# Kernel tuning notes

Measured on AMD Instinct MI355X. Metric: run time of the kernel, lower is better.

The kernel has to match this reference:

```python
import jax, jax.numpy as jnp
import numpy as np

NX = 65536   # spatial cells
T = 32       # time points
H = 128      # MLP hidden width
DX = 1.0     # spatial resolution (init kwarg dx)
S0, S1 = -1.0, 1.0  # fixed stencil (learn_stencil=False)


def setup_inputs() -> dict:
    key = jax.random.key(0)
    k1, k2, k3, k4 = jax.random.split(key, 4)
    t = jnp.arange(T, dtype=jnp.float32) * 0.01          # time grid, dt=0.01
    u0 = jax.random.uniform(k1, (NX,), jnp.float32)      # initial state
    inv_sqrt_h = jnp.float32(1.0 / np.sqrt(H))
    W1 = jax.random.normal(k2, (1, H), jnp.float32)
    W2 = jax.random.normal(k3, (H, H), jnp.float32) * inv_sqrt_h
    W3 = jax.random.normal(k4, (H, 1), jnp.float32) * inv_sqrt_h
    D = jnp.full((1,), 0.01, jnp.float32)                # diffusion coefficient
    BC = jnp.zeros((2, 1), jnp.float32)                  # Dirichlet BC values
    return {"t": t, "u0": u0, "W1": W1, "W2": W2, "W3": W3, "D": D, "BC": BC}


def _flux(u, W1, W2, W3, D, BC):
    # per-cell MLP (func_nn): Linear->Tanh->Linear->Tanh->Linear, no bias, no sigmoid
    h = jnp.tanh(u[:, None] @ W1)        # [Nx, H]
    h = jnp.tanh(h @ W2)                 # [Nx, H]
    a = (h @ W3)[:, 0]                   # [Nx]
    a_plus = jax.nn.relu(a)
    a_min = -jax.nn.relu(-a)
    d = D[0]
    # left fluxes
    lb = d * (S0 * u[0] + S1 * BC[0, 0]) - a_plus[0] / DX * (-S0 * u[0] - S1 * BC[0, 0])
    ln = d * (S0 * u[1:] + S1 * u[:-1]) - a_plus[1:] / DX * (-S0 * u[1:] - S1 * u[:-1])
    left = jnp.concatenate([lb[None], ln])
    # right fluxes
    rb = d * (S0 * u[-1] + S1 * BC[1, 0]) - a_min[-1] / DX * (S0 * u[-1] + S1 * BC[1, 0])
    rn = d * (S0 * u[:-1] + S1 * u[1:]) - a_min[:-1] / DX * (S0 * u[:-1] + S1 * u[1:])
    right = jnp.concatenate([rn, rb[None]])
    return left + right


def reference(t, u0, W1, W2, W3, D, BC):
    # Neural-ODE integration of du/dt = flux_kernel(u); fixed-step RK4 over grid t
    f = lambda u: _flux(u, W1, W2, W3, D, BC)

    def step(u, dt):
        k1 = f(u)
        k2 = f(u + 0.5 * dt * k1)
        k3 = f(u + 0.5 * dt * k2)
        k4 = f(u + dt * k3)
        un = u + (dt / 6.0) * (k1 + 2.0 * k2 + 2.0 * k3 + k4)
        return un, un

    _, us = jax.lax.scan(step, u0, jnp.diff(t))
    return jnp.concatenate([u0[None], us], axis=0)  # [T, Nx]
```

## Files before the change

### kernel.cpp

```cpp
#include <hip/hip_runtime.h>

#define NXC 65536
#define TT 32
#define HH 128
#define TABN 6145
#define TABNP 6146
#define TABLO (-1.0f)
#define TABINV 2048.0f
#define OUTW 32
#define VC 2
#define WINW 128
#define HALO 48

typedef __attribute__((ext_vector_type(8))) short bf16x8;
typedef __attribute__((ext_vector_type(4))) float f32x4;
typedef unsigned short u16;

__device__ __forceinline__ float bf2f(u16 b) {
    union { unsigned int u; float f; } v; v.u = ((unsigned int)b) << 16; return v.f;
}
__device__ __forceinline__ u16 f2bf(float f) {
    union { float f; unsigned int u; } v; v.f = f;
    return (u16)((v.u + 0x7fffu + ((v.u >> 16) & 1u)) >> 16);
}
__device__ __forceinline__ bool is_bf16_mode(const void* t) {
    return ((const u16*)t)[1] != 0;
}

#if __has_builtin(__builtin_amdgcn_exp2f)
#define EXP2F(x) __builtin_amdgcn_exp2f(x)
#else
#define EXP2F(x) exp2f(x)
#endif
#if __has_builtin(__builtin_amdgcn_rcpf)
#define RCPF(x) __builtin_amdgcn_rcpf(x)
#else
#define RCPF(x) (1.0f / (x))
#endif

__device__ __forceinline__ float fast_tanh(float x) {
    float e = EXP2F(x * 2.8853900817779268f);
    return 1.0f - 2.0f * RCPF(e + 1.0f);
}

__global__ __launch_bounds__(256) void tabbuild_kernel(
    const void* traw, const void* W1, const void* W2, const void* W3,
    float* __restrict__ atab) {
    __shared__ __align__(16) u16 w2s[HH * HH];
    __shared__ float w1s[HH];
    __shared__ float w3s[HH];
    bool bf = is_bf16_mode(traw);
    int tid = threadIdx.x;
    if (tid < HH)
        w1s[tid] = bf ? bf2f(((const u16*)W1)[tid]) : ((const float*)W1)[tid];
    else
        w3s[tid - HH] = bf ? bf2f(((const u16*)W3)[tid - HH])
                           : ((const float*)W3)[tid - HH];
#pragma unroll 4
    for (int it = 0; it < (HH * HH) / 256; ++it) {
        int idx = it * 256 + tid;
        u16 b = bf ? ((const u16*)W2)[idx] : f2bf(((const float*)W2)[idx]);
        int k = idx >> 7, n = idx & 127;
        int frag = ((n >> 4) * 4 + (k >> 5)) * 64 + ((k >> 3) & 3) * 16 + (n & 15);
        w2s[(frag << 3) | (k & 7)] = b;
    }
    __syncthreads();

    int lane = tid & 63;
    int wave = tid >> 6;
    int q = lane >> 4;
    int m = lane & 15;
    int base = (blockIdx.x * 4 + wave) * 16;
    float uin = TABLO + (float)(base + m) * (1.0f / TABINV);

    bf16x8 afrag[4];
#pragma unroll
    for (int ks = 0; ks < 4; ++ks)
#pragma unroll
        for (int j = 0; j < 8; ++j) {
            float h = fast_tanh(uin * w1s[ks * 32 + q * 8 + j]);
            afrag[ks][j] = (short)f2bf(h);
        }

    const bf16x8* w2f = (const bf16x8*)w2s;
    float p0 = 0.f, p1 = 0.f, p2 = 0.f, p3 = 0.f;
#pragma unroll
    for (int nt = 0; nt < 8; ++nt) {
        f32x4 acc = {0.f, 0.f, 0.f, 0.f};
#pragma unroll
        for (int ks = 0; ks < 4; ++ks) {
            bf16x8 b = w2f[(nt * 4 + ks) * 64 + lane];
            acc = __builtin_amdgcn_mfma_f32_16x16x32_bf16(afrag[ks], b, acc, 0, 0, 0);
        }
        float w3v = w3s[nt * 16 + m];
        p0 += fast_tanh(acc[0]) * w3v;
        p1 += fast_tanh(acc[1]) * w3v;
        p2 += fast_tanh(acc[2]) * w3v;
        p3 += fast_tanh(acc[3]) * w3v;
    }
#pragma unroll
    for (int sh = 1; sh < 16; sh <<= 1) {
        p0 += __shfl_xor(p0, sh, 64);
        p1 += __shfl_xor(p1, sh, 64);
        p2 += __shfl_xor(p2, sh, 64);
        p3 += __shfl_xor(p3, sh, 64);
    }
    int r = m & 3;
    float a = (r == 0) ? p0 : (r == 1) ? p1 : (r == 2) ? p2 : p3;
    if (m < 4) {
        int e = base + q * 4 + r;
        if (e < TABNP) atab[e] = a;
    }
}

__global__ __launch_bounds__(256) void chunk_kernel(
    const void* traw, const void* uin, float* __restrict__ uout,
    const void* Draw, const void* BCraw, const float* __restrict__ atab,
    void* outbase, int s0, int nsteps) {
    __shared__ __align__(16) float2 tab[TABN];
    __shared__ float t32s[TT];

    int tid = threadIdx.x;
    bool bf = is_bf16_mode(traw);

    for (int e = tid * 4; e < TABN - 1; e += 1024) {
        float4 qv = *(const float4*)(atab + e);
        float nx = atab[e + 4];
        float4 lo = make_float4(qv.x, qv.y - qv.x, qv.y, qv.z - qv.y);
        float4 hi = make_float4(qv.z, qv.w - qv.z, qv.w, nx - qv.w);
        *(float4*)(&tab[e]) = lo;
        *(float4*)(&tab[e + 2]) = hi;
    }
    if (tid == 0)
        tab[TABN - 1] = make_float2(atab[TABN - 1], atab[TABN] - atab[TABN - 1]);
    if (tid < TT)
        t32s[tid] = bf ? bf2f(((const u16*)traw)[tid]) : ((const float*)traw)[tid];

    float d   = bf ? bf2f(((const u16*)Draw)[0])  : ((const float*)Draw)[0];
    float bc0 = bf ? bf2f(((const u16*)BCraw)[0]) : ((const float*)BCraw)[0];
    float bc1 = bf ? bf2f(((const u16*)BCraw)[1]) : ((const float*)BCraw)[1];

    int lane = tid & 63;
    int wid = blockIdx.x * 4 + (tid >> 6);
    int gb = wid * OUTW - HALO + lane * VC;
    int i0 = lane * VC;
    bool first = (s0 == 0);
    bool ownw = (i0 >= HALO) && (i0 < HALO + OUTW);

    float v[VC], ub[VC], kv[VC], kacc[VC];
    bool gok[VC];
#pragma unroll
    for (int j = 0; j < VC; ++j) {
        int g = gb + j;
        gok[j] = (g >= 0) && (g < NXC);
        float x;
        if (first) {
            if (bf) {
                u16 raw = gok[j] ? ((const u16*)uin)[g] : (u16)0;
                x = bf2f(raw);
                if (ownw) ((u16*)outbase)[g] = raw;
            } else {
                float raw = gok[j] ? ((const float*)uin)[g] : 0.f;
                x = raw;
                if (ownw) ((float*)outbase)[g] = raw;
            }
        } else {
            x = gok[j] ? ((const float*)uin)[g] : 0.f;
        }
        if (!gok[j]) x = (g < 0) ? bc0 : bc1;
        v[j] = x;
        ub[j] = x;
    }
    __syncthreads();

    for (int st = 0; st < nsteps; ++st) {
        int step = s0 + st;
        float dt = t32s[step + 1] - t32s[step];
        float dt2 = 0.5f * dt, dt6 = dt * (1.0f / 6.0f);
#pragma unroll
        for (int j = 0; j < VC; ++j) kacc[j] = 0.f;
#pragma unroll
        for (int s = 0; s < 4; ++s) {
            float cnext = (s < 2) ? dt2 : dt;
            float wgt = (s == 1 || s == 2) ? 2.f : 1.f;
            float vup = __shfl_up(v[VC - 1], 1, 64);
            float vdn = __shfl_down(v[0], 1, 64);
#pragma unroll
            for (int j = 0; j < VC; ++j) {
                float vc = v[j];
                float vl = (j == 0) ? vup : v[j - 1];
                float vr = (j == VC - 1) ? vdn : v[j + 1];
                float f = fmaf(vc, TABINV, (-TABLO) * TABINV);
                f = fminf(fmaxf(f, 0.0f), (float)(TABN - 1));
                int e0 = (int)f;
                float frac = f - (float)e0;
                float2 ts = tab[e0];
                float a = fmaf(frac, ts.y, ts.x);
                float ap = fmaxf(a, 0.f);
                float am = fminf(a, 0.f);
                kv[j] = (vl - vc) * (d + ap) + (vr - vc) * (d - am);
            }
#pragma unroll
            for (int j = 0; j < VC; ++j) {
                kacc[j] += wgt * kv[j];
                float nv = (s < 3) ? fmaf(cnext, kv[j], ub[j])
                                   : fmaf(dt6, kacc[j], ub[j]);
                if (gok[j]) {
                    v[j] = nv;
                    if (s == 3) ub[j] = nv;
                }
            }
        }
        long long rb = (long long)(step + 1) * NXC + gb;
        if (ownw) {
            if (bf) {
                unsigned int pk = (unsigned int)f2bf(ub[0])
                                | ((unsigned int)f2bf(ub[1]) << 16);
                *(unsigned int*)&((u16*)outbase)[rb] = pk;
            } else {
                *(float2*)&((float*)outbase)[rb] = make_float2(ub[0], ub[1]);
            }
        }
    }
    if (uout != nullptr && ownw)
        *(float2*)&uout[gb] = make_float2(ub[0], ub[1]);
}

extern "C" void kernel_launch(void* const* d_in, const int* in_sizes, int n_in,
                              void* d_out, int out_size, void* d_ws,
                              size_t ws_size, hipStream_t stream) {
    const void* t  = d_in[0];
    const void* u0 = d_in[1];
    const void* W1 = d_in[2];
    const void* W2 = d_in[3];
    const void* W3 = d_in[4];
    const void* Dp = d_in[5];
    const void* BC = d_in[6];

    float* atab = (float*)d_ws;
    float* uA = atab + TABNP + 2;
    float* uB = uA + NXC;

    tabbuild_kernel<<<(TABNP + 63) / 64, 256, 0, stream>>>(t, W1, W2, W3, atab);

    const int grid = NXC / (OUTW * 4);
    chunk_kernel<<<grid, 256, 0, stream>>>(t, u0, uB, Dp, BC, atab, d_out, 0, 12);
    chunk_kernel<<<grid, 256, 0, stream>>>(t, uB, uA, Dp, BC, atab, d_out, 12, 12);
    chunk_kernel<<<grid, 256, 0, stream>>>(t, uA, nullptr, Dp, BC, atab, d_out, 24, 7);
}
```

Before: 118.3 us.

## Fuse table build and all RK4 steps into one cooperative kernel

Replaces the table-build kernel and three chunked RK4 kernels with a single cooperative launch. Two grid-wide syncs separate the W2 fragment swizzle (now staged through global memory), the table build and the time stepping. The halo grows to 128 cells per side so all 31 steps run without exchanging state between blocks, with 5 cells per lane and 64 owned outputs per wave. This removes three kernel launches and the intermediate state round-trips, at the cost of more redundant halo computation, more registers, and element-wise rather than vectorised output stores.

```diff
diff --git a/kernel.cpp b/kernel.cpp
--- a/kernel.cpp
+++ b/kernel.cpp
@@ -1,4 +1,7 @@
 #include <hip/hip_runtime.h>
+#include <hip/hip_cooperative_groups.h>
+
+namespace cg = cooperative_groups;
 
 #define NXC 65536
 #define TT 32
@@ -7,10 +10,13 @@
 #define TABNP 6146
 #define TABLO (-1.0f)
 #define TABINV 2048.0f
-#define OUTW 32
-#define VC 2
-#define WINW 128
-#define HALO 48
+#define OUTW 64
+#define VC 5
+#define WINW 320
+#define HALO 128
+#define NSTEPS 31
+#define SWZB 64
+#define TABB 97
 
 typedef __attribute__((ext_vector_type(8))) short bf16x8;
 typedef __attribute__((ext_vector_type(4))) float f32x4;
@@ -43,85 +49,118 @@
     return 1.0f - 2.0f * RCPF(e + 1.0f);
 }
 
-__global__ __launch_bounds__(256) void tabbuild_kernel(
-    const void* traw, const void* W1, const void* W2, const void* W3,
-    float* __restrict__ atab) {
-    __shared__ __align__(16) u16 w2s[HH * HH];
+__global__ __launch_bounds__(256) void mega_kernel(
+    const void* traw, const void* u0, const void* W1, const void* W2,
+    const void* W3, const void* Draw, const void* BCraw,
+    u16* __restrict__ w2frag, float* __restrict__ atab,
+    void* __restrict__ outbase) {
+    __shared__ __align__(16) float2 tab[TABN];
+    __shared__ float t32s[TT];
     __shared__ float w1s[HH];
     __shared__ float w3s[HH];
+
+    int tid = threadIdx.x;
     bool bf = is_bf16_mode(traw);
-    int tid = threadIdx.x;
-    if (tid < HH)
-        w1s[tid] = bf ? bf2f(((const u16*)W1)[tid]) : ((const float*)W1)[tid];
-    else
-        w3s[tid - HH] = bf ? bf2f(((const u16*)W3)[tid - HH])
-                           : ((const float*)W3)[tid - HH];
-#pragma unroll 4
-    for (int it = 0; it < (HH * HH) / 256; ++it) {
-        int idx = it * 256 + tid;
-        u16 b = bf ? ((const u16*)W2)[idx] : f2bf(((const float*)W2)[idx]);
-        int k = idx >> 7, n = idx & 127;
-        int frag = ((n >> 4) * 4 + (k >> 5)) * 64 + ((k >> 3) & 3) * 16 + (n & 15);
-        w2s[(frag << 3) | (k & 7)] = b;
-    }
-    __syncthreads();
-
     int lane = tid & 63;
     int wave = tid >> 6;
-    int q = lane >> 4;
-    int m = lane & 15;
-    int base = (blockIdx.x * 4 + wave) * 16;
-    float uin = TABLO + (float)(base + m) * (1.0f / TABINV);
-
-    bf16x8 afrag[4];
-#pragma unroll
-    for (int ks = 0; ks < 4; ++ks)
-#pragma unroll
-        for (int j = 0; j < 8; ++j) {
-            float h = fast_tanh(uin * w1s[ks * 32 + q * 8 + j]);
-            afrag[ks][j] = (short)f2bf(h);
-        }
-
-    const bf16x8* w2f = (const bf16x8*)w2s;
-    float p0 = 0.f, p1 = 0.f, p2 = 0.f, p3 = 0.f;
-#pragma unroll
-    for (int nt = 0; nt < 8; ++nt) {
-        f32x4 acc = {0.f, 0.f, 0.f, 0.f};
-#pragma unroll
-        for (int ks = 0; ks < 4; ++ks) {
-            bf16x8 b = w2f[(nt * 4 + ks) * 64 + lane];
-            acc = __builtin_amdgcn_mfma_f32_16x16x32_bf16(afrag[ks], b, acc, 0, 0, 0);
-        }
-        float w3v = w3s[nt * 16 + m];
-        p0 += fast_tanh(acc[0]) * w3v;
-        p1 += fast_tanh(acc[1]) * w3v;
-        p2 += fast_tanh(acc[2]) * w3v;
-        p3 += fast_tanh(acc[3]) * w3v;
-    }
-#pragma unroll
-    for (int sh = 1; sh < 16; sh <<= 1) {
-        p0 += __shfl_xor(p0, sh, 64);
-        p1 += __shfl_xor(p1, sh, 64);
-        p2 += __shfl_xor(p2, sh, 64);
-        p3 += __shfl_xor(p3, sh, 64);
-    }
-    int r = m & 3;
-    float a = (r == 0) ? p0 : (r == 1) ? p1 : (r == 2) ? p2 : p3;
-    if (m < 4) {
-        int e = base + q * 4 + r;
-        if (e < TABNP) atab[e] = a;
-    }
-}
-
-__global__ __launch_bounds__(256) void chunk_kernel(
-    const void* traw, const void* uin, float* __restrict__ uout,
-    const void* Draw, const void* BCraw, const float* __restrict__ atab,
-    void* outbase, int s0, int nsteps) {
-    __shared__ __align__(16) float2 tab[TABN];
-    __shared__ float t32s[TT];
-
-    int tid = threadIdx.x;
-    bool bf = is_bf16_mode(traw);
+    int wid = blockIdx.x * 4 + wave;
+    int gb = wid * OUTW - HALO + lane * VC;
+    int i0 = lane * VC;
+
+    float d   = bf ? bf2f(((const u16*)Draw)[0])  : ((const float*)Draw)[0];
+    float bc0 = bf ? bf2f(((const u16*)BCraw)[0]) : ((const float*)BCraw)[0];
+    float bc1 = bf ? bf2f(((const u16*)BCraw)[1]) : ((const float*)BCraw)[1];
+
+    float v[VC], ub[VC];
+    bool gok[VC], own[VC];
+#pragma unroll
+    for (int j = 0; j < VC; ++j) {
+        int g = gb + j;
+        int i = i0 + j;
+        gok[j] = (g >= 0) && (g < NXC);
+        own[j] = (i >= HALO) && (i < HALO + OUTW);
+        float x;
+        if (bf) {
+            u16 raw = gok[j] ? ((const u16*)u0)[g] : (u16)0;
+            x = bf2f(raw);
+            if (own[j]) ((u16*)outbase)[g] = raw;
+        } else {
+            float raw = gok[j] ? ((const float*)u0)[g] : 0.f;
+            x = raw;
+            if (own[j]) ((float*)outbase)[g] = raw;
+        }
+        if (!gok[j]) x = (g < 0) ? bc0 : bc1;
+        v[j] = x;
+        ub[j] = x;
+    }
+
+    if (blockIdx.x < SWZB) {
+        int i = blockIdx.x * 256 + tid;
+        int ej = i & 7;
+        int ln = (i >> 3) & 63;
+        int ks = (i >> 9) & 3;
+        int nt = i >> 11;
+        int k = ks * 32 + (ln >> 4) * 8 + ej;
+        int n = nt * 16 + (ln & 15);
+        w2frag[i] = bf ? ((const u16*)W2)[k * HH + n]
+                       : f2bf(((const float*)W2)[k * HH + n]);
+    }
+    cg::this_grid().sync();
+
+    if (blockIdx.x < TABB) {
+        if (tid < HH)
+            w1s[tid] = bf ? bf2f(((const u16*)W1)[tid]) : ((const float*)W1)[tid];
+        else
+            w3s[tid - HH] = bf ? bf2f(((const u16*)W3)[tid - HH])
+                               : ((const float*)W3)[tid - HH];
+        __syncthreads();
+
+        int q = lane >> 4;
+        int m = lane & 15;
+        int base = (blockIdx.x * 4 + wave) * 16;
+        float uin = TABLO + (float)(base + m) * (1.0f / TABINV);
+
+        bf16x8 afrag[4];
+#pragma unroll
+        for (int ks = 0; ks < 4; ++ks)
+#pragma unroll
+            for (int j = 0; j < 8; ++j) {
+                float h = fast_tanh(uin * w1s[ks * 32 + q * 8 + j]);
+                afrag[ks][j] = (short)f2bf(h);
+            }
+
+        const bf16x8* w2f = (const bf16x8*)w2frag;
+        float p0 = 0.f, p1 = 0.f, p2 = 0.f, p3 = 0.f;
+#pragma unroll
+        for (int nt = 0; nt < 8; ++nt) {
+            f32x4 acc = {0.f, 0.f, 0.f, 0.f};
+#pragma unroll
+            for (int ks = 0; ks < 4; ++ks) {
+                bf16x8 b = w2f[(nt * 4 + ks) * 64 + lane];
+                acc = __builtin_amdgcn_mfma_f32_16x16x32_bf16(afrag[ks], b, acc,
+                                                              0, 0, 0);
+            }
+            float w3v = w3s[nt * 16 + m];
+            p0 += fast_tanh(acc[0]) * w3v;
+            p1 += fast_tanh(acc[1]) * w3v;
+            p2 += fast_tanh(acc[2]) * w3v;
+            p3 += fast_tanh(acc[3]) * w3v;
+        }
+#pragma unroll
+        for (int sh = 1; sh < 16; sh <<= 1) {
+            p0 += __shfl_xor(p0, sh, 64);
+            p1 += __shfl_xor(p1, sh, 64);
+            p2 += __shfl_xor(p2, sh, 64);
+            p3 += __shfl_xor(p3, sh, 64);
+        }
+        int r = m & 3;
+        float a = (r == 0) ? p0 : (r == 1) ? p1 : (r == 2) ? p2 : p3;
+        if (m < 4) {
+            int e = base + q * 4 + r;
+            if (e < TABNP) atab[e] = a;
+        }
+    }
+    cg::this_grid().sync();
 
     for (int e = tid * 4; e < TABN - 1; e += 1024) {
         float4 qv = *(const float4*)(atab + e);
@@ -135,48 +174,12 @@
         tab[TABN - 1] = make_float2(atab[TABN - 1], atab[TABN] - atab[TABN - 1]);
     if (tid < TT)
         t32s[tid] = bf ? bf2f(((const u16*)traw)[tid]) : ((const float*)traw)[tid];
-
-    float d   = bf ? bf2f(((const u16*)Draw)[0])  : ((const float*)Draw)[0];
-    float bc0 = bf ? bf2f(((const u16*)BCraw)[0]) : ((const float*)BCraw)[0];
-    float bc1 = bf ? bf2f(((const u16*)BCraw)[1]) : ((const float*)BCraw)[1];
-
-    int lane = tid & 63;
-    int wid = blockIdx.x * 4 + (tid >> 6);
-    int gb = wid * OUTW - HALO + lane * VC;
-    int i0 = lane * VC;
-    bool first = (s0 == 0);
-    bool ownw = (i0 >= HALO) && (i0 < HALO + OUTW);
-
-    float v[VC], ub[VC], kv[VC], kacc[VC];
-    bool gok[VC];
-#pragma unroll
-    for (int j = 0; j < VC; ++j) {
-        int g = gb + j;
-        gok[j] = (g >= 0) && (g < NXC);
-        float x;
-        if (first) {
-            if (bf) {
-                u16 raw = gok[j] ? ((const u16*)uin)[g] : (u16)0;
-                x = bf2f(raw);
-                if (ownw) ((u16*)outbase)[g] = raw;
-            } else {
-                float raw = gok[j] ? ((const float*)uin)[g] : 0.f;
-                x = raw;
-                if (ownw) ((float*)outbase)[g] = raw;
-            }
-        } else {
-            x = gok[j] ? ((const float*)uin)[g] : 0.f;
-        }
-        if (!gok[j]) x = (g < 0) ? bc0 : bc1;
-        v[j] = x;
-        ub[j] = x;
-    }
     __syncthreads();
 
-    for (int st = 0; st < nsteps; ++st) {
-        int step = s0 + st;
-        float dt = t32s[step + 1] - t32s[step];
+    for (int st = 0; st < NSTEPS; ++st) {
+        float dt = t32s[st + 1] - t32s[st];
         float dt2 = 0.5f * dt, dt6 = dt * (1.0f / 6.0f);
+        float kacc[VC], kv[VC];
 #pragma unroll
         for (int j = 0; j < VC; ++j) kacc[j] = 0.f;
 #pragma unroll
@@ -211,19 +214,18 @@
                 }
             }
         }
-        long long rb = (long long)(step + 1) * NXC + gb;
-        if (ownw) {
-            if (bf) {
-                unsigned int pk = (unsigned int)f2bf(ub[0])
-                                | ((unsigned int)f2bf(ub[1]) << 16);
-                *(unsigned int*)&((u16*)outbase)[rb] = pk;
-            } else {
-                *(float2*)&((float*)outbase)[rb] = make_float2(ub[0], ub[1]);
-            }
-        }
-    }
-    if (uout != nullptr && ownw)
-        *(float2*)&uout[gb] = make_float2(ub[0], ub[1]);
+        if (bf) {
+            u16* orow = (u16*)outbase + (size_t)(st + 1) * NXC;
+#pragma unroll
+            for (int j = 0; j < VC; ++j)
+                if (own[j]) orow[gb + j] = f2bf(ub[j]);
+        } else {
+            float* orow = (float*)outbase + (size_t)(st + 1) * NXC;
+#pragma unroll
+            for (int j = 0; j < VC; ++j)
+                if (own[j]) orow[gb + j] = ub[j];
+        }
+    }
 }
 
 extern "C" void kernel_launch(void* const* d_in, const int* in_sizes, int n_in,
@@ -238,13 +240,14 @@
     const void* BC = d_in[6];
 
     float* atab = (float*)d_ws;
-    float* uA = atab + TABNP + 2;
-    float* uB = uA + NXC;
-
-    tabbuild_kernel<<<(TABNP + 63) / 64, 256, 0, stream>>>(t, W1, W2, W3, atab);
+    u16* w2frag = (u16*)(atab + TABNP + 2);
+    void* outb = d_out;
+
+    void* kargs[] = {(void*)&t,  (void*)&u0, (void*)&W1, (void*)&W2,
+                     (void*)&W3, (void*)&Dp, (void*)&BC, (void*)&w2frag,
+                     (void*)&atab, (void*)&outb};
 
     const int grid = NXC / (OUTW * 4);
-    chunk_kernel<<<grid, 256, 0, stream>>>(t, u0, uB, Dp, BC, atab, d_out, 0, 12);
-    chunk_kernel<<<grid, 256, 0, stream>>>(t, uB, uA, Dp, BC, atab, d_out, 12, 12);
-    chunk_kernel<<<grid, 256, 0, stream>>>(t, uA, nullptr, Dp, BC, atab, d_out, 24, 7);
-}
+    hipLaunchCooperativeKernel((void*)mega_kernel, dim3(grid), dim3(256),
+                               kargs, 0, stream);
+}
```

After: 181.2 us. 53.2% more time.

## Widen chunk window to block-level with LDS edge exchange, fewer chunk launches

Applied to the files above, without the earlier changes.

The chunk kernel now treats a whole 256-thread block as one window, with one cell per thread: 128 owned cells and a 64-cell halo on each side. Cells at wave edges are passed between waves through shared memory, with a __syncthreads on every RK stage. This cuts the number of time chunks from three launches to two (16+15 steps) and lowers halo overhead per owned cell. The table-build kernel also stops staging W2 in LDS and reads its fragments straight from global memory. The trade-off is per-stage block barriers and scalar stores where there were paired vector stores.

```diff
diff --git a/kernel.cpp b/kernel.cpp
--- a/kernel.cpp
+++ b/kernel.cpp
@@ -7,10 +7,9 @@
 #define TABNP 6146
 #define TABLO (-1.0f)
 #define TABINV 2048.0f
-#define OUTW 32
-#define VC 2
-#define WINW 128
-#define HALO 48
+#define OWNB 128
+#define WINB 256
+#define HALOB 64
 
 typedef __attribute__((ext_vector_type(8))) short bf16x8;
 typedef __attribute__((ext_vector_type(4))) float f32x4;
@@ -46,7 +45,6 @@
 __global__ __launch_bounds__(256) void tabbuild_kernel(
     const void* traw, const void* W1, const void* W2, const void* W3,
     float* __restrict__ atab) {
-    __shared__ __align__(16) u16 w2s[HH * HH];
     __shared__ float w1s[HH];
     __shared__ float w3s[HH];
     bool bf = is_bf16_mode(traw);
@@ -56,14 +54,6 @@
     else
         w3s[tid - HH] = bf ? bf2f(((const u16*)W3)[tid - HH])
                            : ((const float*)W3)[tid - HH];
-#pragma unroll 4
-    for (int it = 0; it < (HH * HH) / 256; ++it) {
-        int idx = it * 256 + tid;
-        u16 b = bf ? ((const u16*)W2)[idx] : f2bf(((const float*)W2)[idx]);
-        int k = idx >> 7, n = idx & 127;
-        int frag = ((n >> 4) * 4 + (k >> 5)) * 64 + ((k >> 3) & 3) * 16 + (n & 15);
-        w2s[(frag << 3) | (k & 7)] = b;
-    }
     __syncthreads();
 
     int lane = tid & 63;
@@ -82,14 +72,20 @@
             afrag[ks][j] = (short)f2bf(h);
         }
 
-    const bf16x8* w2f = (const bf16x8*)w2s;
+    const u16* w2u = (const u16*)W2;
+    const float* w2ff = (const float*)W2;
     float p0 = 0.f, p1 = 0.f, p2 = 0.f, p3 = 0.f;
 #pragma unroll
     for (int nt = 0; nt < 8; ++nt) {
         f32x4 acc = {0.f, 0.f, 0.f, 0.f};
 #pragma unroll
         for (int ks = 0; ks < 4; ++ks) {
-            bf16x8 b = w2f[(nt * 4 + ks) * 64 + lane];
+            int idx0 = (ks * 32 + q * 8) * HH + nt * 16 + m;
+            bf16x8 b;
+#pragma unroll
+            for (int j = 0; j < 8; ++j)
+                b[j] = bf ? (short)w2u[idx0 + j * HH]
+                          : (short)f2bf(w2ff[idx0 + j * HH]);
             acc = __builtin_amdgcn_mfma_f32_16x16x32_bf16(afrag[ks], b, acc, 0, 0, 0);
         }
         float w3v = w3s[nt * 16 + m];
@@ -116,9 +112,11 @@
 __global__ __launch_bounds__(256) void chunk_kernel(
     const void* traw, const void* uin, float* __restrict__ uout,
     const void* Draw, const void* BCraw, const float* __restrict__ atab,
-    void* outbase, int s0, int nsteps) {
+    void* __restrict__ outbase, int s0, int nsteps) {
     __shared__ __align__(16) float2 tab[TABN];
     __shared__ float t32s[TT];
+    __shared__ float eL[2][4];
+    __shared__ float eR[2][4];
 
     int tid = threadIdx.x;
     bool bf = is_bf16_mode(traw);
@@ -141,35 +139,31 @@
     float bc1 = bf ? bf2f(((const u16*)BCraw)[1]) : ((const float*)BCraw)[1];
 
     int lane = tid & 63;
-    int wid = blockIdx.x * 4 + (tid >> 6);
-    int gb = wid * OUTW - HALO + lane * VC;
-    int i0 = lane * VC;
+    int w = tid >> 6;
+    int g = blockIdx.x * OWNB - HALOB + tid;
+    bool gok = (g >= 0) && (g < NXC);
+    bool own = (tid >= HALOB) && (tid < HALOB + OWNB);
     bool first = (s0 == 0);
-    bool ownw = (i0 >= HALO) && (i0 < HALO + OUTW);
-
-    float v[VC], ub[VC], kv[VC], kacc[VC];
-    bool gok[VC];
-#pragma unroll
-    for (int j = 0; j < VC; ++j) {
-        int g = gb + j;
-        gok[j] = (g >= 0) && (g < NXC);
+
+    float v, ub;
+    {
         float x;
         if (first) {
             if (bf) {
-                u16 raw = gok[j] ? ((const u16*)uin)[g] : (u16)0;
+                u16 raw = gok ? ((const u16*)uin)[g] : (u16)0;
                 x = bf2f(raw);
-                if (ownw) ((u16*)outbase)[g] = raw;
+                if (own) ((u16*)outbase)[g] = raw;
             } else {
-                float raw = gok[j] ? ((const float*)uin)[g] : 0.f;
+                float raw = gok ? ((const float*)uin)[g] : 0.f;
                 x = raw;
-                if (ownw) ((float*)outbase)[g] = raw;
+                if (own) ((float*)outbase)[g] = raw;
             }
         } else {
-            x = gok[j] ? ((const float*)uin)[g] : 0.f;
-        }
-        if (!gok[j]) x = (g < 0) ? bc0 : bc1;
-        v[j] = x;
-        ub[j] = x;
+            x = gok ? ((const float*)uin)[g] : 0.f;
+        }
+        if (!gok) x = (g < 0) ? bc0 : bc1;
+        v = x;
+        ub = x;
     }
     __syncthreads();
 
@@ -177,53 +171,42 @@
         int step = s0 + st;
         float dt = t32s[step + 1] - t32s[step];
         float dt2 = 0.5f * dt, dt6 = dt * (1.0f / 6.0f);
-#pragma unroll
-        for (int j = 0; j < VC; ++j) kacc[j] = 0.f;
+        float kacc = 0.f;
 #pragma unroll
         for (int s = 0; s < 4; ++s) {
+            int p = s & 1;
             float cnext = (s < 2) ? dt2 : dt;
             float wgt = (s == 1 || s == 2) ? 2.f : 1.f;
-            float vup = __shfl_up(v[VC - 1], 1, 64);
-            float vdn = __shfl_down(v[0], 1, 64);
-#pragma unroll
-            for (int j = 0; j < VC; ++j) {
-                float vc = v[j];
-                float vl = (j == 0) ? vup : v[j - 1];
-                float vr = (j == VC - 1) ? vdn : v[j + 1];
-                float f = fmaf(vc, TABINV, (-TABLO) * TABINV);
-                f = fminf(fmaxf(f, 0.0f), (float)(TABN - 1));
-                int e0 = (int)f;
-                float frac = f - (float)e0;
-                float2 ts = tab[e0];
-                float a = fmaf(frac, ts.y, ts.x);
-                float ap = fmaxf(a, 0.f);
-                float am = fminf(a, 0.f);
-                kv[j] = (vl - vc) * (d + ap) + (vr - vc) * (d - am);
+            if (lane == 63) eR[p][w] = v;
+            if (lane == 0)  eL[p][w] = v;
+            __syncthreads();
+            float vl = __shfl_up(v, 1, 64);
+            float vr = __shfl_down(v, 1, 64);
+            if (lane == 0)  vl = (w > 0) ? eR[p][w - 1] : v;
+            if (lane == 63) vr = (w < 3) ? eL[p][w + 1] : v;
+            float f = fmaf(v, TABINV, (-TABLO) * TABINV);
+            f = fminf(fmaxf(f, 0.0f), (float)(TABN - 1));
+            int e0 = (int)f;
+            float frac = f - (float)e0;
+            float2 ts = tab[e0];
+            float a = fmaf(frac, ts.y, ts.x);
+            float ap = fmaxf(a, 0.f);
+            float am = fminf(a, 0.f);
+            float kv = (vl - v) * (d + ap) + (vr - v) * (d - am);
+            kacc += wgt * kv;
+            float nv = (s < 3) ? fmaf(cnext, kv, ub) : fmaf(dt6, kacc, ub);
+            if (gok) {
+                v = nv;
+                if (s == 3) ub = nv;
             }
-#pragma unroll
-            for (int j = 0; j < VC; ++j) {
-                kacc[j] += wgt * kv[j];
-                float nv = (s < 3) ? fmaf(cnext, kv[j], ub[j])
-                                   : fmaf(dt6, kacc[j], ub[j]);
-                if (gok[j]) {
-                    v[j] = nv;
-                    if (s == 3) ub[j] = nv;
-                }
-            }
-        }
-        long long rb = (long long)(step + 1) * NXC + gb;
-        if (ownw) {
-            if (bf) {
-                unsigned int pk = (unsigned int)f2bf(ub[0])
-                                | ((unsigned int)f2bf(ub[1]) << 16);
-                *(unsigned int*)&((u16*)outbase)[rb] = pk;
-            } else {
-                *(float2*)&((float*)outbase)[rb] = make_float2(ub[0], ub[1]);
-            }
-        }
-    }
-    if (uout != nullptr && ownw)
-        *(float2*)&uout[gb] = make_float2(ub[0], ub[1]);
+        }
+        if (own) {
+            size_t rb = (size_t)(step + 1) * NXC + g;
+            if (bf) ((u16*)outbase)[rb] = f2bf(ub);
+            else    ((float*)outbase)[rb] = ub;
+        }
+    }
+    if (uout != nullptr && own) uout[g] = ub;
 }
 
 extern "C" void kernel_launch(void* const* d_in, const int* in_sizes, int n_in,
@@ -238,13 +221,12 @@
     const void* BC = d_in[6];
 
     float* atab = (float*)d_ws;
-    float* uA = atab + TABNP + 2;
-    float* uB = uA + NXC;
+    float* uB = atab + TABNP + 2;
 
     tabbuild_kernel<<<(TABNP + 63) / 64, 256, 0, stream>>>(t, W1, W2, W3, atab);
 
-    const int grid = NXC / (OUTW * 4);
-    chunk_kernel<<<grid, 256, 0, stream>>>(t, u0, uB, Dp, BC, atab, d_out, 0, 12);
-    chunk_kernel<<<grid, 256, 0, stream>>>(t, uB, uA, Dp, BC, atab, d_out, 12, 12);
-    chunk_kernel<<<grid, 256, 0, stream>>>(t, uA, nullptr, Dp, BC, atab, d_out, 24, 7);
-}
+    chunk_kernel<<<NXC / OWNB, 256, 0, stream>>>(t, u0, uB, Dp, BC, atab,
+                                                 d_out, 0, 16);
+    chunk_kernel<<<NXC / OWNB, 256, 0, stream>>>(t, uB, nullptr, Dp, BC, atab,
+                                                 d_out, 16, 15);
+}
```

New measurement: 155.9 us. +31.7%, slower.
